# Performance work log

Hardware: AMD Instinct MI355X
Metric: run time of the kernel (lower is better)

## Reference

```python
import jax, jax.numpy as jnp
import numpy as np

N_TERMS = 500000
TERM_DIM = 300
N_RELS = 40
REL_DIM = 5
BATCH = 500000


def setup_inputs() -> dict:
    key = jax.random.key(0)
    k1, k2, k3, k4, k5, k6 = jax.random.split(key, 6)
    rels = jax.random.randint(k1, (BATCH,), 0, N_RELS)
    terms_L = jax.random.randint(k2, (BATCH,), 0, N_TERMS)
    terms_R = jax.random.randint(k3, (BATCH,), 0, N_TERMS)
    # learned parameters (nn.Embedding weights + assoc tensor)
    term_table = jax.random.normal(k4, (N_TERMS, TERM_DIM), dtype=jnp.float32) * 0.1
    rel_table = jax.random.normal(k5, (N_RELS, REL_DIM), dtype=jnp.float32) * 0.1
    assoc = jax.random.normal(k6, (REL_DIM, TERM_DIM, TERM_DIM), dtype=jnp.float32) * 0.01
    return {
        "rels": rels,
        "terms_L": terms_L,
        "terms_R": terms_R,
        "term_table": term_table,
        "rel_table": rel_table,
        "assoc": assoc,
    }


def reference(rels, terms_L, terms_R, term_table, rel_table, assoc):
    # Gather embeddings
    r = rel_table[rels]          # [B, 5]
    tL = term_table[terms_L]     # [B, D]
    tR = term_table[terms_R]     # [B, D]
    # Trilinear energy: energy_b = sum_{i,j,k} r[b,i] * assoc[i,j,k] * tL[b,j] * tR[b,k]
    # Contract through the small rank-5 relation axis to avoid the original's
    # [B, D, D] intermediate: tmp is only [B, 5, D].
    tmp = jnp.einsum('bj,rjk->brk', tL, assoc)   # [B, 5, D]
    energy = jnp.einsum('brk,bk,br->b', tmp, tR, r)  # [B]
    return energy
```

## Files before the change

kernel.cpp:

```cpp
#include <hip/hip_runtime.h>
#include <hip/hip_bf16.h>

#define DIMT 300
#define DPAD 320
#define NRELS 40
#define RELD 5
#define TILE_M 64
#define MAX_CHUNKS 8192

typedef __attribute__((ext_vector_type(8))) short bf16x8;
typedef __attribute__((ext_vector_type(4))) float f32x4;

#define DESC_OFF 256
#define SORTED_OFF (DESC_OFF + 3*MAX_CHUNKS)
#define MT_OFF_BYTES(B) ((((size_t)(SORTED_OFF + (B)) * 4) + 255) & ~(size_t)255)

__global__ void k_init(int* cnt) {
    int t = threadIdx.x;
    if (t < 64) cnt[t] = 0;
    if (t < 64) cnt[64 + t] = 0;
    if (t == 0) cnt[128] = 0;
}

__global__ void k_hist(const int* __restrict__ rels, int n, int* cnt) {
    __shared__ int l[NRELS];
    int t = threadIdx.x;
    if (t < NRELS) l[t] = 0;
    __syncthreads();
    int b = blockIdx.x * 256 + t;
    if (b < n) atomicAdd(&l[rels[b]], 1);
    __syncthreads();
    if (t < NRELS && l[t]) atomicAdd(&cnt[t], l[t]);
}

__global__ void k_scan(const int* __restrict__ cnt, int* cursor, int* n_chunks,
                       int* desc_rel, int* desc_start, int* desc_end) {
    __shared__ int offs[NRELS + 1];
    __shared__ int coff[NRELS + 1];
    if (threadIdx.x == 0) {
        int s = 0, c = 0;
        for (int r = 0; r < NRELS; r++) {
            offs[r] = s; s += cnt[r];
            coff[r] = c; c += (cnt[r] + TILE_M - 1) / TILE_M;
        }
        offs[NRELS] = s; coff[NRELS] = c;
        *n_chunks = c;
    }
    __syncthreads();
    if (threadIdx.x < NRELS) cursor[threadIdx.x] = offs[threadIdx.x];
    for (int r = 0; r < NRELS; r++) {
        int nch = (cnt[r] + TILE_M - 1) / TILE_M;
        int cend = offs[r] + cnt[r];
        for (int c = threadIdx.x; c < nch; c += 256) {
            int st = offs[r] + c * TILE_M;
            desc_rel[coff[r] + c] = r;
            desc_start[coff[r] + c] = st;
            desc_end[coff[r] + c] = min(st + TILE_M, cend);
        }
    }
}

__global__ void k_scatter(const int* __restrict__ rels, int n, int* cursor,
                          int* __restrict__ sorted) {
    __shared__ int l[NRELS];
    __shared__ int base[NRELS];
    int t = threadIdx.x;
    if (t < NRELS) l[t] = 0;
    __syncthreads();
    int b = blockIdx.x * 256 + t;
    int r = -1, loc = 0;
    if (b < n) { r = rels[b]; loc = atomicAdd(&l[r], 1); }
    __syncthreads();
    if (t < NRELS && l[t]) base[t] = atomicAdd(&cursor[t], l[t]);
    __syncthreads();
    if (b < n) sorted[base[r] + loc] = b;
}

__global__ void k_build_mt(const float* __restrict__ rel_table,
                           const float* __restrict__ assoc,
                           __hip_bfloat16* __restrict__ Mt) {
    int r = blockIdx.x / 100;
    int t6 = blockIdx.x % 100;
    int tn = (t6 / 10) * 32, tj = (t6 % 10) * 32;
    __shared__ float tile[32][33];
    __shared__ float rw[RELD];
    if (threadIdx.x < RELD) rw[threadIdx.x] = rel_table[r * RELD + threadIdx.x];
    __syncthreads();
    for (int e = threadIdx.x; e < 1024; e += 256) {
        int jl = e >> 5, nl = e & 31;
        int j = tj + jl, n = tn + nl;
        float v = 0.f;
        if (j < DIMT && n < DIMT) {
            #pragma unroll
            for (int i = 0; i < RELD; i++) v += rw[i] * assoc[(i * DIMT + j) * DIMT + n];
        }
        tile[jl][nl] = v;
    }
    __syncthreads();
    for (int e = threadIdx.x; e < 1024; e += 256) {
        int nl = e >> 5, jl = e & 31;
        int n = tn + nl, j = tj + jl;
        Mt[((size_t)r * DPAD + n) * DPAD + j] = __float2bfloat16(tile[jl][nl]);
    }
}

__global__ __launch_bounds__(256) void k_gemm(
    const int* __restrict__ sorted, const int* __restrict__ desc_rel,
    const int* __restrict__ desc_start, const int* __restrict__ desc_end,
    const int* __restrict__ n_chunks,
    const int* __restrict__ terms_L, const int* __restrict__ terms_R,
    const float* __restrict__ term_table, const __hip_bfloat16* __restrict__ Mt,
    float* __restrict__ out) {
    int cid = blockIdx.x;
    if (cid >= *n_chunks) return;
    int rel = desc_rel[cid];
    int start = desc_start[cid];
    int tm = desc_end[cid] - start;

    __shared__ __align__(16) __hip_bfloat16 Alds[TILE_M][32];
    __shared__ __align__(16) __hip_bfloat16 Blds[DPAD][32];
    __shared__ int elds[TILE_M];

    int t = threadIdx.x;
    if (t < TILE_M) elds[t] = (t < tm) ? sorted[start + t] : -1;
    __syncthreads();

    int wave = t >> 6, lane = t & 63;
    int quad = lane >> 4, l16 = lane & 15;

    f32x4 acc[20];
    #pragma unroll
    for (int i = 0; i < 20; i++) acc[i] = (f32x4){0.f, 0.f, 0.f, 0.f};

    const __hip_bfloat16* Mtr = Mt + (size_t)rel * DPAD * DPAD;

    int arow = t >> 2, apart = t & 3;
    int ae = elds[arow];
    const float* asrc = (ae >= 0) ? (term_table + (size_t)terms_L[ae] * DIMT) : nullptr;

    for (int kc = 0; kc < 10; kc++) {
        int k0 = kc * 32;
        {
            int kbase = k0 + apart * 8;
            float vals[8];
            if (asrc && kbase + 8 <= DIMT) {
                #pragma unroll
                for (int j = 0; j < 8; j++) vals[j] = asrc[kbase + j];
            } else if (asrc) {
                #pragma unroll
                for (int j = 0; j < 8; j++) vals[j] = (kbase + j < DIMT) ? asrc[kbase + j] : 0.f;
            } else {
                #pragma unroll
                for (int j = 0; j < 8; j++) vals[j] = 0.f;
            }
            __hip_bfloat16* dst = &Alds[arow][apart * 8];
            #pragma unroll
            for (int j = 0; j < 8; j++) dst[j] = __float2bfloat16(vals[j]);
        }
        for (int idx = t; idx < DPAD * 4; idx += 256) {
            int n = idx >> 2, part = idx & 3;
            *((bf16x8*)&Blds[n][part * 8]) =
                *((const bf16x8*)(Mtr + (size_t)n * DPAD + k0 + part * 8));
        }
        __syncthreads();

        bf16x8 afrag = *((const bf16x8*)&Alds[wave * 16 + l16][quad * 8]);
        #pragma unroll
        for (int nt = 0; nt < 20; nt++) {
            bf16x8 bfrag = *((const bf16x8*)&Blds[nt * 16 + l16][quad * 8]);
            acc[nt] = __builtin_amdgcn_mfma_f32_16x16x32_bf16(afrag, bfrag, acc[nt], 0, 0, 0);
        }
        __syncthreads();
    }

    #pragma unroll
    for (int reg = 0; reg < 4; reg++) {
        int mrow = wave * 16 + quad * 4 + reg;
        int e = elds[mrow];
        float s = 0.f;
        if (e >= 0) {
            const float* tr = term_table + (size_t)terms_R[e] * DIMT;
            #pragma unroll
            for (int nt = 0; nt < 20; nt++) {
                int n = nt * 16 + l16;
                if (n < DIMT) s += acc[nt][reg] * tr[n];
            }
        }
        s += __shfl_xor(s, 1);
        s += __shfl_xor(s, 2);
        s += __shfl_xor(s, 4);
        s += __shfl_xor(s, 8);
        if (l16 == 0 && e >= 0) out[e] = s;
    }
}

extern "C" void kernel_launch(void* const* d_in, const int* in_sizes, int n_in,
                              void* d_out, int out_size, void* d_ws, size_t ws_size,
                              hipStream_t stream) {
    const int*   rels       = (const int*)d_in[0];
    const int*   terms_L    = (const int*)d_in[1];
    const int*   terms_R    = (const int*)d_in[2];
    const float* term_table = (const float*)d_in[3];
    const float* rel_table  = (const float*)d_in[4];
    const float* assoc      = (const float*)d_in[5];
    float* out = (float*)d_out;
    int B = in_sizes[0];

    int* wsi        = (int*)d_ws;
    int* cnt        = wsi;
    int* cursor     = wsi + 64;
    int* n_chunks   = wsi + 128;
    int* desc_rel   = wsi + DESC_OFF;
    int* desc_start = desc_rel + MAX_CHUNKS;
    int* desc_end   = desc_start + MAX_CHUNKS;
    int* sorted     = wsi + SORTED_OFF;
    __hip_bfloat16* Mt = (__hip_bfloat16*)((char*)d_ws + MT_OFF_BYTES(B));

    int nb = (B + 255) / 256;
    k_init<<<1, 128, 0, stream>>>(cnt);
    k_hist<<<nb, 256, 0, stream>>>(rels, B, cnt);
    k_scan<<<1, 256, 0, stream>>>(cnt, cursor, n_chunks, desc_rel, desc_start, desc_end);
    k_scatter<<<nb, 256, 0, stream>>>(rels, B, cursor, sorted);
    k_build_mt<<<NRELS * 100, 256, 0, stream>>>(rel_table, assoc, Mt);
    k_gemm<<<MAX_CHUNKS, 256, 0, stream>>>(sorted, desc_rel, desc_start, desc_end,
                                           n_chunks, terms_L, terms_R, term_table, Mt, out);
}
```

Baseline: 1.239 ms.

## Double-buffer Mt tiles with async LDS loads and keep A fragments in registers

The GEMM kernel now streams the per-relation Mt tiles into a two-slot LDS buffer using global_load_lds. The next k-chunk is issued while MFMAs run on the current one. The gathered term_L rows are loaded once up front with float4 reads and converted directly into register-resident bf16 fragments, which removes the A staging buffer in LDS and its per-iteration sync traffic. Launch bounds now request 3 blocks per CU, which trades register headroom (10 A fragments plus 20 accumulators) for occupancy and may force spills.

```diff
diff --git a/kernel.cpp b/kernel.cpp
--- a/kernel.cpp
+++ b/kernel.cpp
@@ -104,7 +104,13 @@
     }
 }
 
-__global__ __launch_bounds__(256) void k_gemm(
+__device__ inline void async_g2l16(const void* g, void* l) {
+    __builtin_amdgcn_global_load_lds(
+        (const __attribute__((address_space(1))) unsigned int*)g,
+        (__attribute__((address_space(3))) unsigned int*)l, 16, 0, 0);
+}
+
+__global__ __launch_bounds__(256, 3) void k_gemm(
     const int* __restrict__ sorted, const int* __restrict__ desc_rel,
     const int* __restrict__ desc_start, const int* __restrict__ desc_end,
     const int* __restrict__ n_chunks,
@@ -117,8 +123,7 @@
     int start = desc_start[cid];
     int tm = desc_end[cid] - start;
 
-    __shared__ __align__(16) __hip_bfloat16 Alds[TILE_M][32];
-    __shared__ __align__(16) __hip_bfloat16 Blds[DPAD][32];
+    __shared__ __align__(16) __hip_bfloat16 Blds[2][DPAD * 32];
     __shared__ int elds[TILE_M];
 
     int t = threadIdx.x;
@@ -127,48 +132,62 @@
 
     int wave = t >> 6, lane = t & 63;
     int quad = lane >> 4, l16 = lane & 15;
+
+    const __hip_bfloat16* Mtr = Mt + (size_t)rel * DPAD * DPAD;
+
+    auto stage = [&](int kc, int buf) {
+        const char* gb = (const char*)Mtr + kc * 64;
+        char* lb = (char*)&Blds[buf][0];
+        #pragma unroll
+        for (int i = 0; i < 5; i++) {
+            int c = t + i * 256;
+            async_g2l16(gb + (size_t)(c >> 2) * (DPAD * 2) + (c & 3) * 16,
+                        lb + c * 16);
+        }
+    };
+
+    stage(0, 0);
+
+    int arow = wave * 16 + l16;
+    int ae = elds[arow];
+    const float* arp = (ae >= 0) ? (term_table + (size_t)terms_L[ae] * DIMT) : nullptr;
+    bf16x8 afrag[10];
+    #pragma unroll
+    for (int kc = 0; kc < 10; kc++) {
+        int kb = kc * 32 + quad * 8;
+        float v[8];
+        if (arp && kb + 8 <= DIMT) {
+            float4 p0 = *(const float4*)(arp + kb);
+            float4 p1 = *(const float4*)(arp + kb + 4);
+            v[0] = p0.x; v[1] = p0.y; v[2] = p0.z; v[3] = p0.w;
+            v[4] = p1.x; v[5] = p1.y; v[6] = p1.z; v[7] = p1.w;
+        } else if (arp) {
+            #pragma unroll
+            for (int j = 0; j < 8; j++) v[j] = (kb + j < DIMT) ? arp[kb + j] : 0.f;
+        } else {
+            #pragma unroll
+            for (int j = 0; j < 8; j++) v[j] = 0.f;
+        }
+        union { bf16x8 v8; __hip_bfloat16 h[8]; } u;
+        #pragma unroll
+        for (int j = 0; j < 8; j++) u.h[j] = __float2bfloat16(v[j]);
+        afrag[kc] = u.v8;
+    }
 
     f32x4 acc[20];
     #pragma unroll
     for (int i = 0; i < 20; i++) acc[i] = (f32x4){0.f, 0.f, 0.f, 0.f};
 
-    const __hip_bfloat16* Mtr = Mt + (size_t)rel * DPAD * DPAD;
-
-    int arow = t >> 2, apart = t & 3;
-    int ae = elds[arow];
-    const float* asrc = (ae >= 0) ? (term_table + (size_t)terms_L[ae] * DIMT) : nullptr;
+    __syncthreads();
 
     for (int kc = 0; kc < 10; kc++) {
-        int k0 = kc * 32;
-        {
-            int kbase = k0 + apart * 8;
-            float vals[8];
-            if (asrc && kbase + 8 <= DIMT) {
-                #pragma unroll
-                for (int j = 0; j < 8; j++) vals[j] = asrc[kbase + j];
-            } else if (asrc) {
-                #pragma unroll
-                for (int j = 0; j < 8; j++) vals[j] = (kbase + j < DIMT) ? asrc[kbase + j] : 0.f;
-            } else {
-                #pragma unroll
-                for (int j = 0; j < 8; j++) vals[j] = 0.f;
-            }
-            __hip_bfloat16* dst = &Alds[arow][apart * 8];
-            #pragma unroll
-            for (int j = 0; j < 8; j++) dst[j] = __float2bfloat16(vals[j]);
-        }
-        for (int idx = t; idx < DPAD * 4; idx += 256) {
-            int n = idx >> 2, part = idx & 3;
-            *((bf16x8*)&Blds[n][part * 8]) =
-                *((const bf16x8*)(Mtr + (size_t)n * DPAD + k0 + part * 8));
-        }
-        __syncthreads();
-
-        bf16x8 afrag = *((const bf16x8*)&Alds[wave * 16 + l16][quad * 8]);
+        int cur = kc & 1;
+        if (kc < 9) stage(kc + 1, cur ^ 1);
+        const __hip_bfloat16* bb = &Blds[cur][0];
         #pragma unroll
         for (int nt = 0; nt < 20; nt++) {
-            bf16x8 bfrag = *((const bf16x8*)&Blds[nt * 16 + l16][quad * 8]);
-            acc[nt] = __builtin_amdgcn_mfma_f32_16x16x32_bf16(afrag, bfrag, acc[nt], 0, 0, 0);
+            bf16x8 bfrag = *((const bf16x8*)(bb + (nt * 16 + l16) * 32 + quad * 8));
+            acc[nt] = __builtin_amdgcn_mfma_f32_16x16x32_bf16(afrag[kc], bfrag, acc[nt], 0, 0, 0);
         }
         __syncthreads();
     }
```

New measurement: 1.070 ms. 13.6% less time.
